# Kernel tuning notes

Hardware: AMD Instinct MI355X
Metric: run time of the kernel (lower is better)

Reference implementation:

```python
import jax, jax.numpy as jnp
import numpy as np

N_AST, M, C, D, H, OUT = 200000, 400000, 25000, 256, 4, 256


def setup_inputs() -> dict:
    key = jax.random.key(0)
    ks = jax.random.split(key, 12)
    s = 0.02
    return {
        "ast_nodes_encodings": jax.random.normal(ks[0], (N_AST, D), jnp.float32),
        "ast_node_idx_to_pdg_node_idx_mapping_key": jax.random.randint(ks[1], (M,), 0, N_AST),
        "ast_node_idx_to_pdg_node_idx_mapping_value": jax.random.randint(ks[2], (M,), 0, C),
        "pdg_node_idx_to_sub_ast_root_idx_mapping_key": jax.random.randint(ks[3], (C,), 0, C),
        "pdg_node_idx_to_sub_ast_root_idx_mapping_value": jax.random.randint(ks[4], (C,), 0, N_AST),
        "nr_cfg_nodes": C,
        "Wq": jax.random.normal(ks[5], (D, D), jnp.float32) * s,
        "bq": jnp.zeros((D,), jnp.float32),
        "Wk": jax.random.normal(ks[6], (D, D), jnp.float32) * s,
        "bk": jnp.zeros((D,), jnp.float32),
        "Wv": jax.random.normal(ks[7], (D, D), jnp.float32) * s,
        "bv": jnp.zeros((D,), jnp.float32),
        "Wo": jax.random.normal(ks[8], (D, OUT), jnp.float32) * s,
        "bo": jnp.zeros((OUT,), jnp.float32),
    }


def _scatter_attn(x, attn_keys, seg, num_segments, Wq, bq, Wk, bk, Wv, bv, Wo, bo):
    # x: [M, D] scattered inputs; attn_keys: [C, D] per-segment queries; seg: [M] segment ids.
    d_h = D // H
    q = (attn_keys @ Wq + bq).reshape(num_segments, H, d_h)  # [C,H,dh]
    k = (x @ Wk + bk).reshape(-1, H, d_h)                    # [M,H,dh]
    v = (x @ Wv + bv).reshape(-1, H, d_h)                    # [M,H,dh]
    scale = 1.0 / jnp.sqrt(jnp.asarray(d_h, x.dtype))
    scores = jnp.einsum('mhd,mhd->mh', k, q[seg]) * scale    # [M,H]
    m = jax.ops.segment_max(scores, seg, num_segments=num_segments)  # [C,H]
    e = jnp.exp(scores - m[seg])                             # [M,H]
    denom = jax.ops.segment_sum(e, seg, num_segments=num_segments)  # [C,H]
    num = jax.ops.segment_sum((e[..., None] * v).reshape(-1, H * d_h),
                              seg, num_segments=num_segments)        # [C,D]
    pooled = (num.reshape(num_segments, H, d_h) / (denom[..., None] + 1e-9)).reshape(num_segments, D)
    return pooled @ Wo + bo                                  # [C,OUT]


def reference(ast_nodes_encodings,
              ast_node_idx_to_pdg_node_idx_mapping_key,
              ast_node_idx_to_pdg_node_idx_mapping_value,
              pdg_node_idx_to_sub_ast_root_idx_mapping_key,
              pdg_node_idx_to_sub_ast_root_idx_mapping_value,
              nr_cfg_nodes, Wq, bq, Wk, bk, Wv, bv, Wo, bo):
    # Build per-CFG-node attention keys: gather sub-AST-root encodings, scatter by PDG node idx.
    root_enc = ast_nodes_encodings[pdg_node_idx_to_sub_ast_root_idx_mapping_value]  # [C,D]
    attn_keys = jnp.zeros((nr_cfg_nodes, D), ast_nodes_encodings.dtype)
    attn_keys = attn_keys.at[pdg_node_idx_to_sub_ast_root_idx_mapping_key].set(root_enc)
    # Gather AST node encodings per mapping entry and attention-pool per CFG node.
    scattered = ast_nodes_encodings[ast_node_idx_to_pdg_node_idx_mapping_key]       # [M,D]
    return _scatter_attn(scattered, attn_keys, ast_node_idx_to_pdg_node_idx_mapping_value,
                         nr_cfg_nodes, Wq, bq, Wk, bk, Wv, bv, Wo, bo)
```

## Files before the change

kernel.cpp:

```cpp
#include <hip/hip_runtime.h>
#include <hip/hip_bf16.h>
#include <math.h>

#define D 256
#define H 4
#define DH 64
#define NOUT 256

typedef short bf16x8 __attribute__((ext_vector_type(8)));
typedef float f32x4 __attribute__((ext_vector_type(4)));

__device__ __forceinline__ ushort f2bf(float f){
  uint b = __float_as_uint(f);
  b += 0x7FFF + ((b >> 16) & 1);
  return (ushort)(b >> 16);
}
__device__ __forceinline__ float bf2f(ushort u){
  return __uint_as_float(((uint)u) << 16);
}

__device__ __forceinline__ float redux32(float v){
  int t;
  t = __builtin_amdgcn_update_dpp(0, __float_as_int(v), 0x121, 0xF, 0xF, true); v += __int_as_float(t);
  t = __builtin_amdgcn_update_dpp(0, __float_as_int(v), 0x122, 0xF, 0xF, true); v += __int_as_float(t);
  t = __builtin_amdgcn_update_dpp(0, __float_as_int(v), 0x124, 0xF, 0xF, true); v += __int_as_float(t);
  t = __builtin_amdgcn_update_dpp(0, __float_as_int(v), 0x128, 0xF, 0xF, true); v += __int_as_float(t);
  v += __shfl_xor(v, 16, 64);
  return v;
}

__global__ void count_winner_kernel(const int* __restrict__ seg, int* __restrict__ counts,
                                    const int* __restrict__ pdgkey, int* __restrict__ winner,
                                    int M, int C){
  int i = blockIdx.x*256 + threadIdx.x;
  if (i < M){ int s = seg[i]; if (s >= 0 && s < C) atomicAdd(&counts[s], 1); }
  if (i < C){ int t = pdgkey[i]; if (t >= 0 && t < C) atomicMax(&winner[t], i); }
}

__global__ __launch_bounds__(1024) void scan1_kernel(const int* __restrict__ counts,
    int* __restrict__ loc, int* __restrict__ btot, int C){
  __shared__ int wtot[16];
  __shared__ int wexcl[16];
  int tid = threadIdx.x, lane = tid & 63, wv = tid >> 6;
  int i = blockIdx.x*1024 + tid;
  int v = (i < C) ? counts[i] : 0;
  int x = v;
  #pragma unroll
  for (int d2 = 1; d2 < 64; d2 <<= 1){
    int t = __shfl_up(x, d2, 64);
    if (lane >= d2) x += t;
  }
  if (lane == 63) wtot[wv] = x;
  __syncthreads();
  if (wv == 0 && lane < 16){
    int t = wtot[lane]; int y = t;
    #pragma unroll
    for (int d2 = 1; d2 < 16; d2 <<= 1){
      int u = __shfl_up(y, d2, 64);
      if (lane >= d2) y += u;
    }
    wexcl[lane] = y - t;
    if (lane == 15) btot[blockIdx.x] = y;
  }
  __syncthreads();
  if (i < C) loc[i] = wexcl[wv] + x - v;
}

__global__ void scan2_kernel(const int* __restrict__ btot, int* __restrict__ bexcl,
                             int nb, int* __restrict__ offsets, int C){
  int lane = threadIdx.x;
  int v = (lane < nb) ? btot[lane] : 0;
  int x = v;
  #pragma unroll
  for (int d2 = 1; d2 < 64; d2 <<= 1){
    int t = __shfl_up(x, d2, 64);
    if (lane >= d2) x += t;
  }
  if (lane < nb) bexcl[lane] = x - v;
  if (lane == 63) offsets[C] = x;
}

__global__ void scan3_kernel(const int* __restrict__ loc, const int* __restrict__ bexcl,
                             int* __restrict__ offsets, int* __restrict__ pos, int C){
  int i = blockIdx.x*256 + threadIdx.x;
  if (i < C){ int o = loc[i] + bexcl[i >> 10]; offsets[i] = o; pos[i] = o; }
}

__global__ void fill_kernel(const int* __restrict__ seg, const int* __restrict__ astkey,
                            int* __restrict__ pos, int* __restrict__ rows, int M, int C){
  int i = blockIdx.x*256 + threadIdx.x;
  if (i < M){
    int s = seg[i];
    if (s >= 0 && s < C){ int p = atomicAdd(&pos[s], 1); rows[p] = astkey[i]; }
  }
}

__global__ __launch_bounds__(256) void prep_weights(
    const float* __restrict__ Wq, const float* __restrict__ Wk,
    const float* __restrict__ Wv, const float* __restrict__ Wo,
    const float* __restrict__ bq, const float* __restrict__ bk,
    const float* __restrict__ bv,
    ushort* __restrict__ Wq16, ushort* __restrict__ Wk16, ushort* __restrict__ Wv16,
    ushort* __restrict__ WoT16,
    float* __restrict__ wqbk, float* __restrict__ bvo,
    float* __restrict__ bqk, float* __restrict__ cbh){
  __shared__ float t[64][65];
  int bid = blockIdx.x, tid = threadIdx.x;
  if (bid < 256){
    int id = bid*256 + tid;
    Wq16[id] = f2bf(Wq[id]);
    Wk16[id] = f2bf(Wk[id]);
    Wv16[id] = f2bf(Wv[id]);
  } else if (bid < 269){
    int id = (bid - 256)*256 + tid;
    if (id < 1024){
      int h = id >> 8, k = id & 255;
      float s = 0.f;
      for (int d = 0; d < DH; d++) s += Wq[(size_t)k*256 + h*64 + d] * bk[h*64 + d];
      wqbk[id] = s;
    } else if (id < 2048){
      int tt = id - 1024; int h = tt >> 8, o = tt & 255;
      float s = 0.f;
      for (int d = 0; d < DH; d++) s += bv[h*64 + d] * Wo[(size_t)(h*64 + d)*256 + o];
      bvo[tt] = s;
    } else if (id < 3072){
      int tt = id - 2048; int h = tt >> 8, e = tt & 255;
      float s = 0.f;
      for (int d = 0; d < DH; d++) s += bq[h*64 + d] * Wk[(size_t)e*256 + h*64 + d];
      bqk[tt] = s;
    } else if (id < 3076){
      int h = id - 3072;
      float s = 0.f;
      for (int d = 0; d < DH; d++) s += bq[h*64 + d] * bk[h*64 + d];
      cbh[h] = s;
    }
  } else {
    int b2 = bid - 269;
    int bx = b2 & 3, by = b2 >> 2;
    int r = tid >> 6, cc = tid & 63;
    #pragma unroll
    for (int rr = 0; rr < 64; rr += 4)
      t[rr + r][cc] = Wo[(size_t)(by*64 + rr + r)*256 + bx*64 + cc];
    __syncthreads();
    #pragma unroll
    for (int rr = 0; rr < 64; rr += 4)
      WoT16[(size_t)(bx*64 + rr + r)*256 + by*64 + cc] = f2bf(t[cc][rr + r]);
  }
}

__global__ void gather_ag(const float* __restrict__ enc, const int* __restrict__ rootval,
                          const int* __restrict__ winner,
                          const float* __restrict__ wqbk, const float* __restrict__ cbh,
                          ushort* __restrict__ Ag, float* __restrict__ qb, int C){
  int id = blockIdx.x*256 + threadIdx.x;
  int c = id >> 6, g = id & 63;
  if (c >= C) return;
  int w = winner[c];
  float4 v = make_float4(0.f, 0.f, 0.f, 0.f);
  if (w >= 0) v = *(const float4*)(enc + (size_t)rootval[w]*D + g*4);
  ushort4 u; u.x = f2bf(v.x); u.y = f2bf(v.y); u.z = f2bf(v.z); u.w = f2bf(v.w);
  *(ushort4*)(Ag + (size_t)c*D + g*4) = u;
  float b0 = bf2f(u.x), b1 = bf2f(u.y), b2 = bf2f(u.z), b3 = bf2f(u.w);
  float pv[4];
  #pragma unroll
  for (int h = 0; h < 4; h++){
    float4 wv = *(const float4*)(wqbk + h*256 + g*4);
    float p = b0*wv.x + b1*wv.y + b2*wv.z + b3*wv.w;
    p = redux32(p);
    p += __shfl_xor(p, 32, 64);
    pv[h] = p;
  }
  if (g < 4) qb[c*4 + g] = pv[g] + cbh[g];
}

template<bool OUT_BF16>
__global__ __launch_bounds__(256) void mfma_gemm(
    const ushort* __restrict__ A, int sA, int acol_h,
    const ushort* __restrict__ Bt, int sBt, int btrow_h, int btcol_h,
    void* __restrict__ Out, int sOut, int outrow_h, int outcol_h,
    int M, int K,
    const float* __restrict__ bias, const float* __restrict__ beta4,
    const float* __restrict__ bvo4){
  __shared__ __align__(16) ushort As[64][72];
  __shared__ __align__(16) ushort Bs[64][72];
  int tid = threadIdx.x;
  int hz = blockIdx.z;
  int m0 = blockIdx.x*64;
  int acol0  = acol_h*hz;
  int btrow0 = blockIdx.y*64 + btrow_h*hz;
  int btcol0 = btcol_h*hz;
  int outrow0 = outrow_h*hz;
  int outcol0 = blockIdx.y*64 + outcol_h*hz;
  int w = tid >> 6, lane = tid & 63, quad = lane >> 4, l16 = lane & 15;
  int r1 = tid >> 3, c8 = (tid & 7)*8;
  f32x4 acc[4] = {};
  for (int k0 = 0; k0 < K; k0 += 64){
    const ushort* ga = A + (size_t)(m0 + r1)*sA + acol0 + k0 + c8;
    uint4 v1 = make_uint4(0,0,0,0), v2 = make_uint4(0,0,0,0);
    if (m0 + r1 < M)      v1 = *(const uint4*)ga;
    if (m0 + r1 + 32 < M) v2 = *(const uint4*)(ga + (size_t)32*sA);
    *(uint4*)&As[r1][c8]      = v1;
    *(uint4*)&As[r1+32][c8]   = v2;
    const ushort* gb = Bt + (size_t)(btrow0 + r1)*sBt + btcol0 + k0 + c8;
    *(uint4*)&Bs[r1][c8]      = *(const uint4*)gb;
    *(uint4*)&Bs[r1+32][c8]   = *(const uint4*)(gb + (size_t)32*sBt);
    __syncthreads();
    #pragma unroll
    for (int ks = 0; ks < 2; ks++){
      bf16x8 b = *(const bf16x8*)&Bs[w*16 + l16][ks*32 + quad*8];
      #pragma unroll
      for (int mt = 0; mt < 4; mt++){
        bf16x8 a = *(const bf16x8*)&As[mt*16 + l16][ks*32 + quad*8];
        acc[mt] = __builtin_amdgcn_mfma_f32_16x16x32_bf16(a, b, acc[mt], 0, 0, 0);
      }
    }
    __syncthreads();
  }
  int col = outcol0 + w*16 + l16;
  int bcol = btrow0 + w*16 + l16;
  float bval = bias ? bias[bcol] : 0.f;
  #pragma unroll
  for (int mt = 0; mt < 4; mt++){
    #pragma unroll
    for (int r = 0; r < 4; r++){
      int row = m0 + mt*16 + quad*4 + r;
      if (row < M){
        float v = acc[mt][r] + bval;
        if (bvo4){
          v += beta4[row*4+0]*bvo4[0*256 + bcol] + beta4[row*4+1]*bvo4[1*256 + bcol]
             + beta4[row*4+2]*bvo4[2*256 + bcol] + beta4[row*4+3]*bvo4[3*256 + bcol];
        }
        if (OUT_BF16) ((ushort*)Out)[(size_t)(outrow0 + row)*sOut + col] = f2bf(v);
        else          ((float*)Out)[(size_t)(outrow0 + row)*sOut + col] = v;
      }
    }
  }
}

__global__ __launch_bounds__(256) void seg_attn(const float* __restrict__ enc,
    const int* __restrict__ rows, const int* __restrict__ offsets,
    const ushort* __restrict__ qk16, const float* __restrict__ qb,
    ushort* __restrict__ Shat16, float* __restrict__ beta, int C){
  int lane = threadIdx.x & 63, wave = threadIdx.x >> 6;
  int half = lane >> 5, sl = lane & 31;
  int c = blockIdx.x*8 + wave*2 + half;
  if (c >= C) return;
  float qk[4][8];
  const ushort* qkp = qk16 + (size_t)c*1024 + sl*8;
  #pragma unroll
  for (int h = 0; h < 4; h++){
    uint4 u = *(const uint4*)(qkp + h*256);
    qk[h][0]=__uint_as_float(u.x<<16); qk[h][1]=__uint_as_float(u.x&0xffff0000u);
    qk[h][2]=__uint_as_float(u.y<<16); qk[h][3]=__uint_as_float(u.y&0xffff0000u);
    qk[h][4]=__uint_as_float(u.z<<16); qk[h][5]=__uint_as_float(u.z&0xffff0000u);
    qk[h][6]=__uint_as_float(u.w<<16); qk[h][7]=__uint_as_float(u.w&0xffff0000u);
  }
  float4 qbv = *(const float4*)(qb + (size_t)c*4);
  float qbh[4] = {qbv.x, qbv.y, qbv.z, qbv.w};
  int off = offsets[c];
  int n = offsets[c+1] - off;
  float S[4][8] = {};
  float l[4] = {0.f, 0.f, 0.f, 0.f};
  int hbase = half*32;
  for (int base = 0; base < n; base += 32){
    int cnt = min(32, n - base);
    int xrow = 0;
    if (sl < cnt) xrow = rows[off + base + sl];
    float4 x0[4], x1[4];
    #pragma unroll
    for (int m = 0; m < 4; m++){
      int idx = (m < cnt) ? m : (cnt - 1);
      int r = __shfl(xrow, hbase + idx, 64);
      const float* p = enc + (size_t)r*256 + sl*8;
      x0[m] = *(const float4*)p;
      x1[m] = *(const float4*)(p + 4);
    }
    for (int j = 0; j < cnt; j += 4){
      float4 n0[4], n1[4];
      #pragma unroll
      for (int m = 0; m < 4; m++){ n0[m] = x0[m]; n1[m] = x1[m]; }
      if (j + 4 < cnt){
        #pragma unroll
        for (int m = 0; m < 4; m++){
          int k = j + 4 + m; k = (k < cnt) ? k : (cnt - 1);
          int r = __shfl(xrow, hbase + k, 64);
          const float* p = enc + (size_t)r*256 + sl*8;
          n0[m] = *(const float4*)p;
          n1[m] = *(const float4*)(p + 4);
        }
      }
      float pm[4][4];
      #pragma unroll
      for (int m = 0; m < 4; m++){
        #pragma unroll
        for (int h = 0; h < 4; h++){
          pm[m][h] = x0[m].x*qk[h][0] + x0[m].y*qk[h][1] + x0[m].z*qk[h][2] + x0[m].w*qk[h][3]
                   + x1[m].x*qk[h][4] + x1[m].y*qk[h][5] + x1[m].z*qk[h][6] + x1[m].w*qk[h][7];
        }
      }
      #pragma unroll
      for (int m = 0; m < 4; m++){
        #pragma unroll
        for (int h = 0; h < 4; h++) pm[m][h] = redux32(pm[m][h]);
      }
      #pragma unroll
      for (int m = 0; m < 4; m++){
        bool valid = (j + m) < cnt;
        #pragma unroll
        for (int h = 0; h < 4; h++)
          pm[m][h] = valid ? __expf((pm[m][h] + qbh[h]) * 0.125f) : 0.f;
      }
      #pragma unroll
      for (int h = 0; h < 4; h++)
        l[h] += (pm[0][h] + pm[1][h]) + (pm[2][h] + pm[3][h]);
      #pragma unroll
      for (int m = 0; m < 4; m++){
        #pragma unroll
        for (int h = 0; h < 4; h++){
          float e = pm[m][h];
          S[h][0] += e*x0[m].x; S[h][1] += e*x0[m].y;
          S[h][2] += e*x0[m].z; S[h][3] += e*x0[m].w;
          S[h][4] += e*x1[m].x; S[h][5] += e*x1[m].y;
          S[h][6] += e*x1[m].z; S[h][7] += e*x1[m].w;
        }
      }
      #pragma unroll
      for (int m = 0; m < 4; m++){ x0[m] = n0[m]; x1[m] = n1[m]; }
    }
  }
  float inv[4];
  #pragma unroll
  for (int h = 0; h < 4; h++) inv[h] = 1.f / (l[h] + 1e-9f);
  ushort* sp = Shat16 + (size_t)c*1024 + sl*8;
  #pragma unroll
  for (int h = 0; h < 4; h++){
    float ih = inv[h];
    uint4 o;
    o.x = (uint)f2bf(S[h][0]*ih) | ((uint)f2bf(S[h][1]*ih) << 16);
    o.y = (uint)f2bf(S[h][2]*ih) | ((uint)f2bf(S[h][3]*ih) << 16);
    o.z = (uint)f2bf(S[h][4]*ih) | ((uint)f2bf(S[h][5]*ih) << 16);
    o.w = (uint)f2bf(S[h][6]*ih) | ((uint)f2bf(S[h][7]*ih) << 16);
    *(uint4*)(sp + h*256) = o;
  }
  if (sl == 0){
    beta[c*4+0] = l[0] / (l[0] + 1e-9f);
    beta[c*4+1] = l[1] / (l[1] + 1e-9f);
    beta[c*4+2] = l[2] / (l[2] + 1e-9f);
    beta[c*4+3] = l[3] / (l[3] + 1e-9f);
  }
}

extern "C" void kernel_launch(void* const* d_in, const int* in_sizes, int n_in,
                              void* d_out, int out_size, void* d_ws, size_t ws_size,
                              hipStream_t stream) {
  const float* enc    = (const float*)d_in[0];
  const int*   astkey = (const int*)d_in[1];
  const int*   seg    = (const int*)d_in[2];
  const int*   pdgkey = (const int*)d_in[3];
  const int*   pdgval = (const int*)d_in[4];
  const float* Wq = (const float*)d_in[6];
  const float* bq = (const float*)d_in[7];
  const float* Wk = (const float*)d_in[8];
  const float* bk = (const float*)d_in[9];
  const float* Wv = (const float*)d_in[10];
  const float* bv = (const float*)d_in[11];
  const float* Wo = (const float*)d_in[12];
  const float* bo = (const float*)d_in[13];
  float* out = (float*)d_out;
  const int M = in_sizes[1];
  const int C = in_sizes[3];

  char* p = (char*)d_ws;
  auto alloc = [&](size_t bytes) -> void* {
    void* r = (void*)p;
    p += (bytes + 255) / 256 * 256;
    return r;
  };
  ushort* Ag      = (ushort*)alloc((size_t)C * D * 2);
  ushort* qk16    = (ushort*)alloc((size_t)C * H * D * 2);
  ushort* Shat16  = (ushort*)alloc((size_t)C * H * D * 2);
  float*  beta    = (float*)alloc((size_t)C * H * 4);
  float*  qb      = (float*)alloc((size_t)C * H * 4);
  ushort* Wq16    = (ushort*)alloc((size_t)D * D * 2);
  ushort* Wk16    = (ushort*)alloc((size_t)D * D * 2);
  ushort* Wv16    = (ushort*)alloc((size_t)D * D * 2);
  ushort* WoT16   = (ushort*)alloc((size_t)D * D * 2);
  ushort* Gt16    = (ushort*)alloc((size_t)H * D * D * 2);
  ushort* Zt16    = (ushort*)alloc((size_t)D * H * D * 2);
  float*  wqbk    = (float*)alloc((size_t)H * D * 4);
  float*  bvo     = (float*)alloc((size_t)H * NOUT * 4);
  float*  bqk     = (float*)alloc((size_t)H * D * 4);
  float*  cbh     = (float*)alloc((size_t)H * 4);
  int*   winner   = (int*)alloc((size_t)C * 4);
  int*   counts   = (int*)alloc((size_t)C * 4);
  int*   loc      = (int*)alloc((size_t)C * 4);
  int*   btot     = (int*)alloc((size_t)64 * 4);
  int*   bexcl    = (int*)alloc((size_t)64 * 4);
  int*   offsets  = (int*)alloc((size_t)(C + 1) * 4);
  int*   pos      = (int*)alloc((size_t)C * 4);
  int*   rows     = (int*)alloc((size_t)M * 4);

  hipMemsetAsync(winner, 0xFF, (size_t)C * 4, stream);
  hipMemsetAsync(counts, 0, (size_t)C * 4, stream);

  int gC = (C + 255) / 256, gM = (M + 255) / 256;
  int gMC = ((M > C ? M : C) + 255) / 256;
  int nb1024 = (C + 1023) / 1024;
  count_winner_kernel<<<gMC, 256, 0, stream>>>(seg, counts, pdgkey, winner, M, C);
  scan1_kernel<<<nb1024, 1024, 0, stream>>>(counts, loc, btot, C);
  scan2_kernel<<<1, 64, 0, stream>>>(btot, bexcl, nb1024, offsets, C);
  scan3_kernel<<<gC, 256, 0, stream>>>(loc, bexcl, offsets, pos, C);
  fill_kernel<<<gM, 256, 0, stream>>>(seg, astkey, pos, rows, M, C);

  prep_weights<<<285, 256, 0, stream>>>(Wq, Wk, Wv, Wo, bq, bk, bv,
                                        Wq16, Wk16, Wv16, WoT16, wqbk, bvo, bqk, cbh);

  mfma_gemm<true><<<dim3(4,4,4), 256, 0, stream>>>(
      Wk16, D, DH,  Wq16, D, 0, DH,  Gt16, D, D, 0,  D, DH, nullptr, nullptr, nullptr);
  mfma_gemm<true><<<dim3(4,4,4), 256, 0, stream>>>(
      WoT16, D, DH,  Wv16, D, 0, DH,  Zt16, H*D, 0, D,  D, DH, nullptr, nullptr, nullptr);

  gather_ag<<<(C*64 + 255)/256, 256, 0, stream>>>(enc, pdgval, winner, wqbk, cbh,
                                                  Ag, qb, C);

  int mt = (C + 63) / 64;
  mfma_gemm<true><<<dim3(mt,4,4), 256, 0, stream>>>(
      Ag, D, 0,  Gt16, D, D, 0,  qk16, H*D, 0, D,  C, D, bqk, nullptr, nullptr);

  seg_attn<<<(C + 7)/8, 256, 0, stream>>>(enc, rows, offsets, qk16, qb,
                                          Shat16, beta, C);

  mfma_gemm<false><<<dim3(mt,4,1), 256, 0, stream>>>(
      Shat16, H*D, 0,  Zt16, H*D, 0, 0,  out, NOUT, 0, 0,  C, H*D, bo, beta, bvo);
}
```

Baseline: 499.1 us.

## Merge setup kernels into fewer launches and use single-block scan

```diff
diff --git a/kernel.cpp b/kernel.cpp
--- a/kernel.cpp
+++ b/kernel.cpp
@@ -29,73 +29,9 @@
   return v;
 }
 
-__global__ void count_winner_kernel(const int* __restrict__ seg, int* __restrict__ counts,
-                                    const int* __restrict__ pdgkey, int* __restrict__ winner,
-                                    int M, int C){
-  int i = blockIdx.x*256 + threadIdx.x;
-  if (i < M){ int s = seg[i]; if (s >= 0 && s < C) atomicAdd(&counts[s], 1); }
-  if (i < C){ int t = pdgkey[i]; if (t >= 0 && t < C) atomicMax(&winner[t], i); }
-}
-
-__global__ __launch_bounds__(1024) void scan1_kernel(const int* __restrict__ counts,
-    int* __restrict__ loc, int* __restrict__ btot, int C){
-  __shared__ int wtot[16];
-  __shared__ int wexcl[16];
-  int tid = threadIdx.x, lane = tid & 63, wv = tid >> 6;
-  int i = blockIdx.x*1024 + tid;
-  int v = (i < C) ? counts[i] : 0;
-  int x = v;
-  #pragma unroll
-  for (int d2 = 1; d2 < 64; d2 <<= 1){
-    int t = __shfl_up(x, d2, 64);
-    if (lane >= d2) x += t;
-  }
-  if (lane == 63) wtot[wv] = x;
-  __syncthreads();
-  if (wv == 0 && lane < 16){
-    int t = wtot[lane]; int y = t;
-    #pragma unroll
-    for (int d2 = 1; d2 < 16; d2 <<= 1){
-      int u = __shfl_up(y, d2, 64);
-      if (lane >= d2) y += u;
-    }
-    wexcl[lane] = y - t;
-    if (lane == 15) btot[blockIdx.x] = y;
-  }
-  __syncthreads();
-  if (i < C) loc[i] = wexcl[wv] + x - v;
-}
-
-__global__ void scan2_kernel(const int* __restrict__ btot, int* __restrict__ bexcl,
-                             int nb, int* __restrict__ offsets, int C){
-  int lane = threadIdx.x;
-  int v = (lane < nb) ? btot[lane] : 0;
-  int x = v;
-  #pragma unroll
-  for (int d2 = 1; d2 < 64; d2 <<= 1){
-    int t = __shfl_up(x, d2, 64);
-    if (lane >= d2) x += t;
-  }
-  if (lane < nb) bexcl[lane] = x - v;
-  if (lane == 63) offsets[C] = x;
-}
-
-__global__ void scan3_kernel(const int* __restrict__ loc, const int* __restrict__ bexcl,
-                             int* __restrict__ offsets, int* __restrict__ pos, int C){
-  int i = blockIdx.x*256 + threadIdx.x;
-  if (i < C){ int o = loc[i] + bexcl[i >> 10]; offsets[i] = o; pos[i] = o; }
-}
-
-__global__ void fill_kernel(const int* __restrict__ seg, const int* __restrict__ astkey,
-                            int* __restrict__ pos, int* __restrict__ rows, int M, int C){
-  int i = blockIdx.x*256 + threadIdx.x;
-  if (i < M){
-    int s = seg[i];
-    if (s >= 0 && s < C){ int p = atomicAdd(&pos[s], 1); rows[p] = astkey[i]; }
-  }
-}
-
-__global__ __launch_bounds__(256) void prep_weights(
+__global__ __launch_bounds__(256) void k1_count_prep(
+    const int* __restrict__ seg, int* __restrict__ counts,
+    const int* __restrict__ pdgkey, int* __restrict__ winner, int M, int C, int nCW,
     const float* __restrict__ Wq, const float* __restrict__ Wk,
     const float* __restrict__ Wv, const float* __restrict__ Wo,
     const float* __restrict__ bq, const float* __restrict__ bk,
@@ -106,13 +42,20 @@
     float* __restrict__ bqk, float* __restrict__ cbh){
   __shared__ float t[64][65];
   int bid = blockIdx.x, tid = threadIdx.x;
-  if (bid < 256){
-    int id = bid*256 + tid;
+  if (bid < nCW){
+    int i = bid*256 + tid;
+    if (i < M){ int s = seg[i]; if (s >= 0 && s < C) atomicAdd(&counts[s], 1); }
+    if (i < C){ int tt = pdgkey[i]; if (tt >= 0 && tt < C) atomicMax(&winner[tt], i); }
+    return;
+  }
+  int b = bid - nCW;
+  if (b < 256){
+    int id = b*256 + tid;
     Wq16[id] = f2bf(Wq[id]);
     Wk16[id] = f2bf(Wk[id]);
     Wv16[id] = f2bf(Wv[id]);
-  } else if (bid < 269){
-    int id = (bid - 256)*256 + tid;
+  } else if (b < 269){
+    int id = (b - 256)*256 + tid;
     if (id < 1024){
       int h = id >> 8, k = id & 255;
       float s = 0.f;
@@ -135,7 +78,7 @@
       cbh[h] = s;
     }
   } else {
-    int b2 = bid - 269;
+    int b2 = b - 269;
     int bx = b2 & 3, by = b2 >> 2;
     int r = tid >> 6, cc = tid & 63;
     #pragma unroll
@@ -148,11 +91,128 @@
   }
 }
 
-__global__ void gather_ag(const float* __restrict__ enc, const int* __restrict__ rootval,
-                          const int* __restrict__ winner,
-                          const float* __restrict__ wqbk, const float* __restrict__ cbh,
-                          ushort* __restrict__ Ag, float* __restrict__ qb, int C){
-  int id = blockIdx.x*256 + threadIdx.x;
+__global__ __launch_bounds__(1024) void scan_all(const int* __restrict__ counts,
+    int* __restrict__ offsets, int* __restrict__ pos, int C){
+  __shared__ int wtot[16];
+  __shared__ int wexcl[16];
+  __shared__ int bt;
+  __shared__ int srun;
+  int tid = threadIdx.x, lane = tid & 63, wv = tid >> 6;
+  if (tid == 0) srun = 0;
+  __syncthreads();
+  int nch = (C + 1023) >> 10;
+  for (int ch = 0; ch < nch; ch++){
+    int i = ch*1024 + tid;
+    int v = (i < C) ? counts[i] : 0;
+    int x = v;
+    #pragma unroll
+    for (int d2 = 1; d2 < 64; d2 <<= 1){
+      int tt = __shfl_up(x, d2, 64);
+      if (lane >= d2) x += tt;
+    }
+    if (lane == 63) wtot[wv] = x;
+    __syncthreads();
+    if (wv == 0 && lane < 16){
+      int tt = wtot[lane]; int y = tt;
+      #pragma unroll
+      for (int d2 = 1; d2 < 16; d2 <<= 1){
+        int u = __shfl_up(y, d2, 64);
+        if (lane >= d2) y += u;
+      }
+      wexcl[lane] = y - tt;
+      if (lane == 15) bt = y;
+    }
+    __syncthreads();
+    if (i < C){ int o = srun + wexcl[wv] + x - v; offsets[i] = o; pos[i] = o; }
+    __syncthreads();
+    if (tid == 0) srun += bt;
+    __syncthreads();
+  }
+  if (tid == 0) offsets[C] = srun;
+}
+
+__device__ __forceinline__ void gemm64_body(
+    ushort (*As)[72], ushort (*Bs)[72],
+    const ushort* __restrict__ A, int sA, int acol_h,
+    const ushort* __restrict__ Bt, int sBt, int btrow_h, int btcol_h,
+    ushort* __restrict__ Out, int sOut, int outrow_h, int outcol_h,
+    int Mr, int K, int bx, int by, int hz, int tid){
+  int m0 = bx*64;
+  int acol0  = acol_h*hz;
+  int btrow0 = by*64 + btrow_h*hz;
+  int btcol0 = btcol_h*hz;
+  int outrow0 = outrow_h*hz;
+  int outcol0 = by*64 + outcol_h*hz;
+  int w = tid >> 6, lane = tid & 63, quad = lane >> 4, l16 = lane & 15;
+  int r1 = tid >> 3, c8 = (tid & 7)*8;
+  f32x4 acc[4] = {};
+  for (int k0 = 0; k0 < K; k0 += 64){
+    const ushort* ga = A + (size_t)(m0 + r1)*sA + acol0 + k0 + c8;
+    uint4 v1 = make_uint4(0,0,0,0), v2 = make_uint4(0,0,0,0);
+    if (m0 + r1 < Mr)      v1 = *(const uint4*)ga;
+    if (m0 + r1 + 32 < Mr) v2 = *(const uint4*)(ga + (size_t)32*sA);
+    *(uint4*)&As[r1][c8]      = v1;
+    *(uint4*)&As[r1+32][c8]   = v2;
+    const ushort* gb = Bt + (size_t)(btrow0 + r1)*sBt + btcol0 + k0 + c8;
+    *(uint4*)&Bs[r1][c8]      = *(const uint4*)gb;
+    *(uint4*)&Bs[r1+32][c8]   = *(const uint4*)(gb + (size_t)32*sBt);
+    __syncthreads();
+    #pragma unroll
+    for (int ks = 0; ks < 2; ks++){
+      bf16x8 bfr = *(const bf16x8*)&Bs[w*16 + l16][ks*32 + quad*8];
+      #pragma unroll
+      for (int mt = 0; mt < 4; mt++){
+        bf16x8 afr = *(const bf16x8*)&As[mt*16 + l16][ks*32 + quad*8];
+        acc[mt] = __builtin_amdgcn_mfma_f32_16x16x32_bf16(afr, bfr, acc[mt], 0, 0, 0);
+      }
+    }
+    __syncthreads();
+  }
+  int col = outcol0 + w*16 + l16;
+  #pragma unroll
+  for (int mt = 0; mt < 4; mt++){
+    #pragma unroll
+    for (int r = 0; r < 4; r++){
+      int row = m0 + mt*16 + quad*4 + r;
+      if (row < Mr)
+        Out[(size_t)(outrow0 + row)*sOut + col] = f2bf(acc[mt][r]);
+    }
+  }
+}
+
+__global__ __launch_bounds__(256) void k3_fill_gemm_gather(
+    const int* __restrict__ seg, const int* __restrict__ astkey,
+    int* __restrict__ pos, int* __restrict__ rows, int M, int nF,
+    const ushort* __restrict__ Wk16, const ushort* __restrict__ Wq16,
+    const ushort* __restrict__ WoT16, const ushort* __restrict__ Wv16,
+    ushort* __restrict__ Gt16, ushort* __restrict__ Zt16,
+    const float* __restrict__ enc, const int* __restrict__ rootval,
+    const int* __restrict__ winner,
+    const float* __restrict__ wqbk, const float* __restrict__ cbh,
+    ushort* __restrict__ Ag, float* __restrict__ qb, int C){
+  __shared__ __align__(16) ushort As[64][72];
+  __shared__ __align__(16) ushort Bs[64][72];
+  int bid = blockIdx.x, tid = threadIdx.x;
+  if (bid < nF){
+    int i = bid*256 + tid;
+    if (i < M){
+      int s = seg[i];
+      if (s >= 0 && s < C){ int p = atomicAdd(&pos[s], 1); rows[p] = astkey[i]; }
+    }
+    return;
+  }
+  if (bid < nF + 128){
+    int b2 = bid - nF;
+    int bx = b2 & 3, by = (b2 >> 2) & 3, hz = b2 >> 4;
+    if (hz < 4)
+      gemm64_body(As, Bs, Wk16, D, DH,  Wq16, D, 0, DH,  Gt16, D, D, 0,
+                  D, DH, bx, by, hz, tid);
+    else
+      gemm64_body(As, Bs, WoT16, D, DH,  Wv16, D, 0, DH,  Zt16, H*D, 0, D,
+                  D, DH, bx, by, hz - 4, tid);
+    return;
+  }
+  int id = (bid - nF - 128)*256 + tid;
   int c = id >> 6, g = id & 63;
   if (c >= C) return;
   int w = winner[c];
@@ -160,12 +220,12 @@
   if (w >= 0) v = *(const float4*)(enc + (size_t)rootval[w]*D + g*4);
   ushort4 u; u.x = f2bf(v.x); u.y = f2bf(v.y); u.z = f2bf(v.z); u.w = f2bf(v.w);
   *(ushort4*)(Ag + (size_t)c*D + g*4) = u;
-  float b0 = bf2f(u.x), b1 = bf2f(u.y), b2 = bf2f(u.z), b3 = bf2f(u.w);
+  float b0 = bf2f(u.x), b1 = bf2f(u.y), b2f = bf2f(u.z), b3 = bf2f(u.w);
   float pv[4];
   #pragma unroll
   for (int h = 0; h < 4; h++){
     float4 wv = *(const float4*)(wqbk + h*256 + g*4);
-    float p = b0*wv.x + b1*wv.y + b2*wv.z + b3*wv.w;
+    float p = b0*wv.x + b1*wv.y + b2f*wv.z + b3*wv.w;
     p = redux32(p);
     p += __shfl_xor(p, 32, 64);
     pv[h] = p;
@@ -393,9 +453,6 @@
   float*  cbh     = (float*)alloc((size_t)H * 4);
   int*   winner   = (int*)alloc((size_t)C * 4);
   int*   counts   = (int*)alloc((size_t)C * 4);
-  int*   loc      = (int*)alloc((size_t)C * 4);
-  int*   btot     = (int*)alloc((size_t)64 * 4);
-  int*   bexcl    = (int*)alloc((size_t)64 * 4);
   int*   offsets  = (int*)alloc((size_t)(C + 1) * 4);
   int*   pos      = (int*)alloc((size_t)C * 4);
   int*   rows     = (int*)alloc((size_t)M * 4);
@@ -403,27 +460,23 @@
   hipMemsetAsync(winner, 0xFF, (size_t)C * 4, stream);
   hipMemsetAsync(counts, 0, (size_t)C * 4, stream);
 
-  int gC = (C + 255) / 256, gM = (M + 255) / 256;
+  int gM = (M + 255) / 256;
   int gMC = ((M > C ? M : C) + 255) / 256;
-  int nb1024 = (C + 1023) / 1024;
-  count_winner_kernel<<<gMC, 256, 0, stream>>>(seg, counts, pdgkey, winner, M, C);
-  scan1_kernel<<<nb1024, 1024, 0, stream>>>(counts, loc, btot, C);
-  scan2_kernel<<<1, 64, 0, stream>>>(btot, bexcl, nb1024, offsets, C);
-  scan3_kernel<<<gC, 256, 0, stream>>>(loc, bexcl, offsets, pos, C);
-  fill_kernel<<<gM, 256, 0, stream>>>(seg, astkey, pos, rows, M, C);
-
-  prep_weights<<<285, 256, 0, stream>>>(Wq, Wk, Wv, Wo, bq, bk, bv,
-                                        Wq16, Wk16, Wv16, WoT16, wqbk, bvo, bqk, cbh);
-
-  mfma_gemm<true><<<dim3(4,4,4), 256, 0, stream>>>(
-      Wk16, D, DH,  Wq16, D, 0, DH,  Gt16, D, D, 0,  D, DH, nullptr, nullptr, nullptr);
-  mfma_gemm<true><<<dim3(4,4,4), 256, 0, stream>>>(
-      WoT16, D, DH,  Wv16, D, 0, DH,  Zt16, H*D, 0, D,  D, DH, nullptr, nullptr, nullptr);
-
-  gather_ag<<<(C*64 + 255)/256, 256, 0, stream>>>(enc, pdgval, winner, wqbk, cbh,
-                                                  Ag, qb, C);
-
+  int gAg = (C*64 + 255) / 256;
   int mt = (C + 63) / 64;
+
+  k1_count_prep<<<gMC + 285, 256, 0, stream>>>(
+      seg, counts, pdgkey, winner, M, C, gMC,
+      Wq, Wk, Wv, Wo, bq, bk, bv,
+      Wq16, Wk16, Wv16, WoT16, wqbk, bvo, bqk, cbh);
+
+  scan_all<<<1, 1024, 0, stream>>>(counts, offsets, pos, C);
+
+  k3_fill_gemm_gather<<<gM + 128 + gAg, 256, 0, stream>>>(
+      seg, astkey, pos, rows, M, gM,
+      Wk16, Wq16, WoT16, Wv16, Gt16, Zt16,
+      enc, pdgval, winner, wqbk, cbh, Ag, qb, C);
+
   mfma_gemm<true><<<dim3(mt,4,4), 256, 0, stream>>>(
       Ag, D, 0,  Gt16, D, D, 0,  qk16, H*D, 0, D,  C, D, bqk, nullptr, nullptr);
 
```

Measured after the change: 506.5 us. About the same (+1.5%).
